# Performance work log

Measured on AMD Instinct MI355X. Metric: run time of the kernel, lower is better.

The kernel has to match this reference:

```python
import jax, jax.numpy as jnp
from jax import lax
import numpy as np

H = W = 2048
C = 3
KSIZE = 2
SIGMA = 2.0
ITERATIONS = 2
RADII = (256.0, 768.0)
# with max_displacement=0 all circle centers coincide, so 'close to any circle'
# reduces to distance^2 < max(radius^2)
SRADII_MAX = max(r ** 2 for r in RADII)
SCLEAN_MAX = max(max(r - KSIZE, 0.0) ** 2 for r in RADII)


def _gaussian_blur(x, sigma):
    """skimage.filters.gaussian equivalent: separable gaussian, truncate=4.0,
    mode='nearest' (edge padding), channel_axis=-1 (no blur across channels)."""
    radius = int(4.0 * sigma + 0.5)
    t = np.arange(-radius, radius + 1, dtype=np.float32)
    k = np.exp(-0.5 * (t / sigma) ** 2)
    k = (k / k.sum()).astype(np.float32)
    for axis in (0, 1):
        pad = [(0, 0)] * x.ndim
        pad[axis] = (radius, radius)
        xp = jnp.pad(x, pad, mode='edge')
        n = x.shape[axis]
        acc = jnp.zeros_like(x)
        for j in range(k.shape[0]):
            acc = acc + k[j] * lax.slice_in_dim(xp, j, j + n, axis=axis)
        x = acc
    return x


def _glass_forward(img, offsets):
    r = KSIZE
    Hv = H - 2 * r + 1  # loop range(r, H-r+1) -> H-2r+1 rows
    Wv = W - 2 * r + 1
    HWtot = H * W
    # original quirk: cx = shape[0]//2 compared against column index w,
    # cy = shape[1]//2 against row index h; identical for a square image.
    cx = H // 2
    cy = W // 2
    ys = jnp.arange(r, H - r + 1)
    xs = jnp.arange(r, W - r + 1)
    HH, WW = jnp.meshgrid(ys, xs, indexing='ij')  # (Hv, Wv)
    d2 = (cx - WW) ** 2 + (cy - HH) ** 2
    swap_mask = (d2 >= SRADII_MAX).reshape(-1)  # swap only OUTSIDE all circles
    local = ((HH - r) * Wv + (WW - r)).reshape(-1)  # raster order within loop
    lin = (HH * W + WW).reshape(-1)

    # Every read in the original swap loop comes from array_orig (never
    # updated), so the final value of each pixel equals array_orig[source]
    # where source is determined by the LAST write targeting that pixel.
    # Each loop step emits two ordered writes:
    #   array[h, w]   = orig[h_, w_]   (order = 2*raster)
    #   array[h_, w_] = orig[h, w]    (order = 2*raster + 1)
    # We replay this exactly with a scatter-max over write order.
    writes = []
    for i in range(ITERATIONS):
        dh = offsets[i, :, :, 0]
        dw = offsets[i, :, :, 1]
        lin_ = ((HH + dh) * W + (WW + dw)).reshape(-1)
        base = i * 2 * Hv * Wv
        o1 = base + 2 * local
        o2 = o1 + 1
        writes.append((lin, lin_, o1))
        writes.append((lin_, lin, o2))

    win = jnp.full((HWtot,), -1, jnp.int32)
    for tgt, src_idx, order in writes:
        win = win.at[tgt].max(jnp.where(swap_mask, order, -1))
    src = jnp.full((HWtot,), -1, jnp.int32)
    for tgt, src_idx, order in writes:
        hit = swap_mask & (order == win[tgt])
        src = src.at[tgt].max(jnp.where(hit, src_idx, -1))

    orig_flat = img.reshape(HWtot, C)
    gathered = orig_flat[jnp.maximum(src, 0)]
    swapped = jnp.where((src >= 0)[:, None], gathered, orig_flat).reshape(H, W, C)

    blurred = jnp.clip(_gaussian_blur(swapped / 255.0, SIGMA), 0.0, 1.0) * 255.0

    # restore original pixels close to the shrunken (clean) circles
    clean = d2 < SCLEAN_MAX  # (Hv, Wv)
    clean_full = jnp.zeros((H, W), bool).at[r:H - r + 1, r:W - r + 1].set(clean)
    return jnp.where(clean_full[:, :, None], img, blurred)


def setup_inputs() -> dict:
    key = jax.random.key(0)
    k1, k2 = jax.random.split(key)
    img = jax.random.uniform(k1, (H, W, C), jnp.float32) * 255.0
    offsets = jax.random.randint(
        k2, (ITERATIONS, H - 2 * KSIZE + 1, W - 2 * KSIZE + 1, 2),
        -KSIZE, KSIZE, dtype=jnp.int32)
    return {"img": img, "offsets": offsets}


def reference(img, offsets):
    return _glass_forward(img, offsets)
```

## Files before the change

### kernel.cpp

```cpp
#include <hip/hip_runtime.h>
#include <hip/hip_fp16.h>

#define Hh 2048
#define Ww 2048
#define HW (2048 * 2048)
constexpr int REG = 2045;
constexpr int RBASE = 2 * 2045 * 2045;
constexpr int SWAP_D2 = 589824;
constexpr int CLEAN_D2 = 586756;

__device__ __constant__ float GK[17] = {
    6.691628e-05f, 4.363490e-04f, 2.215963e-03f, 8.764304e-03f,
    2.699596e-02f, 6.475994e-02f, 1.209875e-01f, 1.760358e-01f,
    1.9947466e-01f, 1.760358e-01f, 1.209875e-01f, 6.475994e-02f,
    2.699596e-02f, 8.764304e-03f, 2.215963e-03f, 4.363490e-04f,
    6.691628e-05f};

constexpr int TX = 32, TY = 8;
constexpr int HX = TX + 3, HY = TY + 3;

__global__ __launch_bounds__(256) void swap_gather(
    const float* __restrict__ img, const int* __restrict__ off,
    __half* __restrict__ A) {
  int x0 = blockIdx.x * TX, y0 = blockIdx.y * TY;
  int tx = threadIdx.x & 31, ty = threadIdx.x >> 5;
  int px = x0 + tx, py = y0 + ty;
  int plin = py * Ww + px;
  int srcoff = 0;

  int mxx = max(abs(1024 - (x0 - 1)), abs(1024 - (x0 + TX + 1)));
  int mxy = max(abs(1024 - (y0 - 1)), abs(1024 - (y0 + TY + 1)));
  if (mxx * mxx + mxy * mxy >= SWAP_D2) {
    __shared__ unsigned sh[HY * HX];
    for (int e = threadIdx.x; e < HY * HX; e += 256) {
      int ly = e / HX, lx = e - ly * HX;
      int qy = y0 - 1 + ly, qx = x0 - 1 + lx;
      unsigned v = 0xFFFFFFFFu;
      int dcx = 1024 - qx, dcy = 1024 - qy;
      if (qy >= 2 && qy <= 2046 && qx >= 2 && qx <= 2046 &&
          dcx * dcx + dcy * dcy >= SWAP_D2) {
        int base = ((qy - 2) * REG + (qx - 2)) * 2;
        const int2 a0 = *(const int2*)&off[base];
        const int2 a1 = *(const int2*)&off[RBASE + base];
        v = (unsigned)(a0.y + 2) | ((unsigned)(a0.x + 2) << 8) |
            ((unsigned)(a1.y + 2) << 16) | ((unsigned)(a1.x + 2) << 24);
      }
      sh[e] = v;
    }
    __syncthreads();

    unsigned w[4][4];
#pragma unroll
    for (int dyi = 0; dyi < 4; ++dyi)
#pragma unroll
      for (int dxi = 0; dxi < 4; ++dxi)
        w[dyi][dxi] = sh[(ty + dyi) * HX + (tx + dxi)];

#define CANDC(dyi, dxi) ((unsigned)((1 - (dxi)) + 2) | ((unsigned)((1 - (dyi)) + 2) << 8))
#define OFFC(dyi, dxi) (-(1 - (dyi)) * Ww - (1 - (dxi)))
#define CAND0(dyi, dxi) \
  if ((w[dyi][dxi] & 0xFFFFu) == CANDC(dyi, dxi)) srcoff = OFFC(dyi, dxi);
#define CAND1(dyi, dxi) \
  if ((w[dyi][dxi] >> 16) == CANDC(dyi, dxi)) srcoff = OFFC(dyi, dxi);

    CAND0(0, 0) CAND0(0, 1) CAND0(0, 2) CAND0(0, 3)
    CAND0(1, 0) CAND0(1, 1) CAND0(1, 2) CAND0(1, 3)
    CAND0(2, 0) CAND0(2, 1) CAND0(2, 2) CAND0(2, 3)
    CAND0(3, 0) CAND0(3, 1) CAND0(3, 2) CAND0(3, 3)
    CAND1(0, 0) CAND1(0, 1) CAND1(0, 2) CAND1(0, 3)
    CAND1(1, 0)
    {
      unsigned wc = w[1][1];
      if ((wc >> 24) != 0xFFu) {
        int dh1 = (int)((wc >> 24) & 0xFFu) - 2;
        int dw1 = (int)((wc >> 16) & 0xFFu) - 2;
        srcoff = dh1 * Ww + dw1;
      }
    }
    CAND1(1, 1) CAND1(1, 2) CAND1(1, 3)
    CAND1(2, 0) CAND1(2, 1) CAND1(2, 2) CAND1(2, 3)
    CAND1(3, 0) CAND1(3, 1) CAND1(3, 2) CAND1(3, 3)
#undef CANDC
#undef OFFC
#undef CAND0
#undef CAND1
  }

  int src = plin + srcoff;
  float r = img[src * 3 + 0];
  float g = img[src * 3 + 1];
  float b = img[src * 3 + 2];
  A[plin] = __float2half(r);
  A[HW + plin] = __float2half(g);
  A[2 * HW + plin] = __float2half(b);
}

constexpr int YPT = 16;
__global__ __launch_bounds__(256) void vblur(const __half* __restrict__ A,
                                             __half* __restrict__ B) {
  int b = blockIdx.x;
  int xcd = b & 7, r = b >> 3;
  int ystrip = (xcd << 4) | (r & 15);
  int rem = r >> 4;
  int xb = rem & 1, c = rem >> 1;
  int x0 = (xb * 256 + threadIdx.x) * 4;
  int y0 = ystrip * YPT;
  const __half* Ap = A + (size_t)c * HW;
  __half* Bp = B + (size_t)c * HW;

  float acc[YPT][4];
#pragma unroll
  for (int k = 0; k < YPT; ++k)
#pragma unroll
    for (int q = 0; q < 4; ++q) acc[k][q] = 0.f;

#pragma unroll
  for (int j = 0; j < YPT + 16; ++j) {
    int ys = y0 - 8 + j;
    ys = ys < 0 ? 0 : (ys > Hh - 1 ? Hh - 1 : ys);
    uint2 raw = *(const uint2*)&Ap[(size_t)ys * Ww + x0];
    __half2 h01 = *(__half2*)&raw.x;
    __half2 h23 = *(__half2*)&raw.y;
    float2 v01 = __half22float2(h01);
    float2 v23 = __half22float2(h23);
#pragma unroll
    for (int k = 0; k < YPT; ++k) {
      int t = j - k;
      if (t >= 0 && t <= 16) {
        float gk = GK[t];
        acc[k][0] += gk * v01.x;
        acc[k][1] += gk * v01.y;
        acc[k][2] += gk * v23.x;
        acc[k][3] += gk * v23.y;
      }
    }
  }
#pragma unroll
  for (int k = 0; k < YPT; ++k) {
    uint2 o;
    __half2 h01 = __float22half2_rn(make_float2(acc[k][0], acc[k][1]));
    __half2 h23 = __float22half2_rn(make_float2(acc[k][2], acc[k][3]));
    o.x = *(unsigned*)&h01;
    o.y = *(unsigned*)&h23;
    *(uint2*)&Bp[(size_t)(y0 + k) * Ww + x0] = o;
  }
}

__global__ __launch_bounds__(256) void hblur_compose(
    const __half* __restrict__ B, const float* __restrict__ img,
    float* __restrict__ out) {
  __shared__ float tile[528 + 1];
  int tid = threadIdx.x;
  int xs = blockIdx.x * 512;
  int y = blockIdx.y;
  float br[3][2];

  for (int c = 0; c < 3; ++c) {
    const __half* Bp = B + (size_t)c * HW + (size_t)y * Ww;
    __syncthreads();
    for (int e = tid; e < 264; e += 256) {
      int xg = xs - 8 + 2 * e;
      float2 v;
      if (xg >= 0 && xg + 1 <= Ww - 1) {
        __half2 h = *(const __half2*)&Bp[xg];
        v = __half22float2(h);
      } else {
        int xlo = xg < 0 ? 0 : (xg > Ww - 1 ? Ww - 1 : xg);
        int xhi = xg + 1 < 0 ? 0 : (xg + 1 > Ww - 1 ? Ww - 1 : xg + 1);
        v = make_float2(__half2float(Bp[xlo]), __half2float(Bp[xhi]));
      }
      *(float2*)&tile[2 * e] = v;
    }
    __syncthreads();
    float f[19];
#pragma unroll
    for (int j = 0; j < 19; ++j) f[j] = tile[2 * tid + j];
    float s0 = 0.f, s1 = 0.f;
#pragma unroll
    for (int j = 0; j < 17; ++j) {
      s0 += GK[j] * f[j];
      s1 += GK[j] * f[j + 1];
    }
    br[c][0] = s0;
    br[c][1] = s1;
  }

  int x = xs + 2 * tid;
#pragma unroll
  for (int u = 0; u < 2; ++u) {
    int xu = x + u;
    int dx = 1024 - xu, dy = 1024 - y;
    bool clean = (xu >= 2 && xu <= 2046 && y >= 2 && y <= 2046 &&
                  dx * dx + dy * dy < CLEAN_D2);
    int p3 = (y * Ww + xu) * 3;
    if (clean) {
      out[p3 + 0] = img[p3 + 0];
      out[p3 + 1] = img[p3 + 1];
      out[p3 + 2] = img[p3 + 2];
    } else {
#pragma unroll
      for (int c = 0; c < 3; ++c) {
        float v = br[c][u];
        v = v < 0.f ? 0.f : (v > 255.f ? 255.f : v);
        out[p3 + c] = v;
      }
    }
  }
}

extern "C" void kernel_launch(void* const* d_in, const int* in_sizes, int n_in,
                              void* d_out, int out_size, void* d_ws,
                              size_t ws_size, hipStream_t stream) {
  const float* img = (const float*)d_in[0];
  const int* off = (const int*)d_in[1];
  float* out = (float*)d_out;

  __half* A = (__half*)d_ws;
  __half* Bp = A + (size_t)3 * HW;

  swap_gather<<<dim3(Ww / TX, Hh / TY), 256, 0, stream>>>(img, off, A);
  vblur<<<768, 256, 0, stream>>>(A, Bp);
  hblur_compose<<<dim3(Ww / 512, Hh), 256, 0, stream>>>(Bp, img, out);
}
```

Measured before the change: 178.9 us.

## Fuse vertical and horizontal blur into one tiled kernel and skip clean tiles

```diff
diff --git a/kernel.cpp b/kernel.cpp
--- a/kernel.cpp
+++ b/kernel.cpp
@@ -8,6 +8,7 @@
 constexpr int RBASE = 2 * 2045 * 2045;
 constexpr int SWAP_D2 = 589824;
 constexpr int CLEAN_D2 = 586756;
+constexpr int SKIP_D2 = 569000;
 
 __device__ __constant__ float GK[17] = {
     6.691628e-05f, 4.363490e-04f, 2.215963e-03f, 8.764304e-03f,
@@ -16,22 +17,31 @@
     2.699596e-02f, 8.764304e-03f, 2.215963e-03f, 4.363490e-04f,
     6.691628e-05f};
 
+__device__ __forceinline__ int clampi(int v, int lo, int hi) {
+  return v < lo ? lo : (v > hi ? hi : v);
+}
+
 constexpr int TX = 32, TY = 8;
 constexpr int HX = TX + 3, HY = TY + 3;
 
 __global__ __launch_bounds__(256) void swap_gather(
     const float* __restrict__ img, const int* __restrict__ off,
     __half* __restrict__ A) {
+  __shared__ unsigned sh[HY * HX];
+  __shared__ __align__(16) float simg[12 * 108];
   int x0 = blockIdx.x * TX, y0 = blockIdx.y * TY;
   int tx = threadIdx.x & 31, ty = threadIdx.x >> 5;
   int px = x0 + tx, py = y0 + ty;
   int plin = py * Ww + px;
-  int srcoff = 0;
-
+
+  int bxx = max(abs(1024 - x0), abs(1024 - (x0 + TX - 1)));
+  int bxy = max(abs(1024 - y0), abs(1024 - (y0 + TY - 1)));
+  if (bxx * bxx + bxy * bxy < SKIP_D2) return;
+
+  float r, g, b;
   int mxx = max(abs(1024 - (x0 - 1)), abs(1024 - (x0 + TX + 1)));
   int mxy = max(abs(1024 - (y0 - 1)), abs(1024 - (y0 + TY + 1)));
   if (mxx * mxx + mxy * mxy >= SWAP_D2) {
-    __shared__ unsigned sh[HY * HX];
     for (int e = threadIdx.x; e < HY * HX; e += 256) {
       int ly = e / HX, lx = e - ly * HX;
       int qy = y0 - 1 + ly, qx = x0 - 1 + lx;
@@ -47,6 +57,23 @@
       }
       sh[e] = v;
     }
+    if (x0 >= 2 && x0 <= 2013) {
+      for (int e = threadIdx.x; e < 648; e += 256) {
+        int rr = e / 54, c2 = e - rr * 54;
+        int qy = clampi(y0 - 2 + rr, 0, 2047);
+        *(float2*)&simg[rr * 108 + 2 * c2] =
+            *(const float2*)&img[(size_t)qy * 6144 + (size_t)(x0 - 2) * 3 +
+                                 2 * c2];
+      }
+    } else {
+      for (int e = threadIdx.x; e < 1296; e += 256) {
+        int rr = e / 108, c3 = e - rr * 108;
+        int col = c3 / 3, ch = c3 - col * 3;
+        int qy = clampi(y0 - 2 + rr, 0, 2047);
+        int qx = clampi(x0 - 2 + col, 0, 2047);
+        simg[e] = img[((size_t)qy * Ww + qx) * 3 + ch];
+      }
+    }
     __syncthreads();
 
     unsigned w[4][4];
@@ -56,12 +83,13 @@
       for (int dxi = 0; dxi < 4; ++dxi)
         w[dyi][dxi] = sh[(ty + dyi) * HX + (tx + dxi)];
 
+    int loff = 0;
 #define CANDC(dyi, dxi) ((unsigned)((1 - (dxi)) + 2) | ((unsigned)((1 - (dyi)) + 2) << 8))
-#define OFFC(dyi, dxi) (-(1 - (dyi)) * Ww - (1 - (dxi)))
+#define LOFFC(dyi, dxi) (-(1 - (dyi)) * 36 - (1 - (dxi)))
 #define CAND0(dyi, dxi) \
-  if ((w[dyi][dxi] & 0xFFFFu) == CANDC(dyi, dxi)) srcoff = OFFC(dyi, dxi);
+  if ((w[dyi][dxi] & 0xFFFFu) == CANDC(dyi, dxi)) loff = LOFFC(dyi, dxi);
 #define CAND1(dyi, dxi) \
-  if ((w[dyi][dxi] >> 16) == CANDC(dyi, dxi)) srcoff = OFFC(dyi, dxi);
+  if ((w[dyi][dxi] >> 16) == CANDC(dyi, dxi)) loff = LOFFC(dyi, dxi);
 
     CAND0(0, 0) CAND0(0, 1) CAND0(0, 2) CAND0(0, 3)
     CAND0(1, 0) CAND0(1, 1) CAND0(1, 2) CAND0(1, 3)
@@ -74,135 +102,124 @@
       if ((wc >> 24) != 0xFFu) {
         int dh1 = (int)((wc >> 24) & 0xFFu) - 2;
         int dw1 = (int)((wc >> 16) & 0xFFu) - 2;
-        srcoff = dh1 * Ww + dw1;
+        loff = dh1 * 36 + dw1;
       }
     }
     CAND1(1, 1) CAND1(1, 2) CAND1(1, 3)
     CAND1(2, 0) CAND1(2, 1) CAND1(2, 2) CAND1(2, 3)
     CAND1(3, 0) CAND1(3, 1) CAND1(3, 2) CAND1(3, 3)
 #undef CANDC
-#undef OFFC
+#undef LOFFC
 #undef CAND0
 #undef CAND1
+
+    int L = ((ty + 2) * 36 + (tx + 2) + loff) * 3;
+    r = simg[L + 0];
+    g = simg[L + 1];
+    b = simg[L + 2];
+  } else {
+    r = img[(size_t)plin * 3 + 0];
+    g = img[(size_t)plin * 3 + 1];
+    b = img[(size_t)plin * 3 + 2];
   }
-
-  int src = plin + srcoff;
-  float r = img[src * 3 + 0];
-  float g = img[src * 3 + 1];
-  float b = img[src * 3 + 2];
   A[plin] = __float2half(r);
   A[HW + plin] = __float2half(g);
   A[2 * HW + plin] = __float2half(b);
 }
 
-constexpr int YPT = 16;
-__global__ __launch_bounds__(256) void vblur(const __half* __restrict__ A,
-                                             __half* __restrict__ B) {
-  int b = blockIdx.x;
-  int xcd = b & 7, r = b >> 3;
-  int ystrip = (xcd << 4) | (r & 15);
-  int rem = r >> 4;
-  int xb = rem & 1, c = rem >> 1;
-  int x0 = (xb * 256 + threadIdx.x) * 4;
-  int y0 = ystrip * YPT;
-  const __half* Ap = A + (size_t)c * HW;
-  __half* Bp = B + (size_t)c * HW;
-
-  float acc[YPT][4];
-#pragma unroll
-  for (int k = 0; k < YPT; ++k)
-#pragma unroll
-    for (int q = 0; q < 4; ++q) acc[k][q] = 0.f;
-
-#pragma unroll
-  for (int j = 0; j < YPT + 16; ++j) {
-    int ys = y0 - 8 + j;
-    ys = ys < 0 ? 0 : (ys > Hh - 1 ? Hh - 1 : ys);
-    uint2 raw = *(const uint2*)&Ap[(size_t)ys * Ww + x0];
-    __half2 h01 = *(__half2*)&raw.x;
-    __half2 h23 = *(__half2*)&raw.y;
-    float2 v01 = __half22float2(h01);
-    float2 v23 = __half22float2(h23);
-#pragma unroll
-    for (int k = 0; k < YPT; ++k) {
-      int t = j - k;
-      if (t >= 0 && t <= 16) {
-        float gk = GK[t];
-        acc[k][0] += gk * v01.x;
-        acc[k][1] += gk * v01.y;
-        acc[k][2] += gk * v23.x;
-        acc[k][3] += gk * v23.y;
-      }
-    }
+constexpr int BTW = 128, BTH = 32;
+constexpr int SW = BTW + 16;
+constexpr int SH = BTH + 16;
+
+__global__ __launch_bounds__(256) void blur_compose(
+    const __half* __restrict__ A, const float* __restrict__ img,
+    float* __restrict__ out) {
+  int lin = blockIdx.x;
+  int swz = (lin & 7) * 128 + (lin >> 3);
+  int tyb = swz & 63, txb = swz >> 6;
+  int x0 = txb * BTW, y0 = tyb * BTH;
+  int tid = threadIdx.x;
+
+  int mxx = max(abs(1024 - x0), abs(1024 - (x0 + BTW - 1)));
+  int mxy = max(abs(1024 - y0), abs(1024 - (y0 + BTH - 1)));
+  if (mxx * mxx + mxy * mxy < CLEAN_D2) {
+    const float4* ip = (const float4*)(img + ((size_t)y0 * Ww + x0) * 3);
+    float4* op = (float4*)(out + ((size_t)y0 * Ww + x0) * 3);
+    for (int e = tid; e < 3072; e += 256) {
+      int rr = e / 96, c4 = e - rr * 96;
+      op[(size_t)rr * 1536 + c4] = ip[(size_t)rr * 1536 + c4];
+    }
+    return;
   }
-#pragma unroll
-  for (int k = 0; k < YPT; ++k) {
-    uint2 o;
-    __half2 h01 = __float22half2_rn(make_float2(acc[k][0], acc[k][1]));
-    __half2 h23 = __float22half2_rn(make_float2(acc[k][2], acc[k][3]));
-    o.x = *(unsigned*)&h01;
-    o.y = *(unsigned*)&h23;
-    *(uint2*)&Bp[(size_t)(y0 + k) * Ww + x0] = o;
-  }
-}
-
-__global__ __launch_bounds__(256) void hblur_compose(
-    const __half* __restrict__ B, const float* __restrict__ img,
-    float* __restrict__ out) {
-  __shared__ float tile[528 + 1];
-  int tid = threadIdx.x;
-  int xs = blockIdx.x * 512;
-  int y = blockIdx.y;
-  float br[3][2];
+
+  __shared__ __align__(16) __half S[SH * SW];
+  __shared__ __align__(8) __half V[BTH * SW];
+
+  bool xin = (x0 >= 8) && (x0 + SW - 8 <= Ww);
 
   for (int c = 0; c < 3; ++c) {
-    const __half* Bp = B + (size_t)c * HW + (size_t)y * Ww;
-    __syncthreads();
-    for (int e = tid; e < 264; e += 256) {
-      int xg = xs - 8 + 2 * e;
-      float2 v;
-      if (xg >= 0 && xg + 1 <= Ww - 1) {
-        __half2 h = *(const __half2*)&Bp[xg];
-        v = __half22float2(h);
-      } else {
-        int xlo = xg < 0 ? 0 : (xg > Ww - 1 ? Ww - 1 : xg);
-        int xhi = xg + 1 < 0 ? 0 : (xg + 1 > Ww - 1 ? Ww - 1 : xg + 1);
-        v = make_float2(__half2float(Bp[xlo]), __half2float(Bp[xhi]));
-      }
-      *(float2*)&tile[2 * e] = v;
-    }
-    __syncthreads();
-    float f[19];
-#pragma unroll
-    for (int j = 0; j < 19; ++j) f[j] = tile[2 * tid + j];
-    float s0 = 0.f, s1 = 0.f;
-#pragma unroll
-    for (int j = 0; j < 17; ++j) {
-      s0 += GK[j] * f[j];
-      s1 += GK[j] * f[j + 1];
-    }
-    br[c][0] = s0;
-    br[c][1] = s1;
-  }
-
-  int x = xs + 2 * tid;
-#pragma unroll
-  for (int u = 0; u < 2; ++u) {
-    int xu = x + u;
-    int dx = 1024 - xu, dy = 1024 - y;
-    bool clean = (xu >= 2 && xu <= 2046 && y >= 2 && y <= 2046 &&
-                  dx * dx + dy * dy < CLEAN_D2);
-    int p3 = (y * Ww + xu) * 3;
-    if (clean) {
-      out[p3 + 0] = img[p3 + 0];
-      out[p3 + 1] = img[p3 + 1];
-      out[p3 + 2] = img[p3 + 2];
+    const __half* Ap = A + (size_t)c * HW;
+    __syncthreads();
+    if (xin) {
+      for (int e = tid; e < SH * 18; e += 256) {
+        int rr = e / 18, ch = e - rr * 18;
+        int ys = clampi(y0 - 8 + rr, 0, Hh - 1);
+        *(uint4*)&S[rr * SW + ch * 8] =
+            *(const uint4*)&Ap[(size_t)ys * Ww + (x0 - 8) + ch * 8];
+      }
     } else {
-#pragma unroll
-      for (int c = 0; c < 3; ++c) {
-        float v = br[c][u];
+      for (int e = tid; e < SH * SW; e += 256) {
+        int rr = e / SW, j = e - rr * SW;
+        int ys = clampi(y0 - 8 + rr, 0, Hh - 1);
+        int xs = clampi(x0 - 8 + j, 0, Ww - 1);
+        S[e] = Ap[(size_t)ys * Ww + xs];
+      }
+    }
+    __syncthreads();
+    for (int e = tid; e < BTH * 72; e += 256) {
+      int rr = e / 72, p = e - rr * 72;
+      float s0 = 0.f, s1 = 0.f;
+#pragma unroll
+      for (int t = 0; t < 17; ++t) {
+        float2 v = __half22float2(*(const __half2*)&S[(rr + t) * SW + 2 * p]);
+        s0 += GK[t] * v.x;
+        s1 += GK[t] * v.y;
+      }
+      *(__half2*)&V[rr * SW + 2 * p] = __float22half2_rn(make_float2(s0, s1));
+    }
+    __syncthreads();
+    for (int e = tid; e < BTH * 64; e += 256) {
+      int rr = e >> 6, xh = e & 63;
+      int x = 2 * xh;
+      float f[18];
+#pragma unroll
+      for (int t = 0; t < 9; ++t) {
+        float2 v = __half22float2(*(const __half2*)&V[rr * SW + x + 2 * t]);
+        f[2 * t] = v.x;
+        f[2 * t + 1] = v.y;
+      }
+      float s0 = 0.f, s1 = 0.f;
+#pragma unroll
+      for (int t = 0; t < 17; ++t) {
+        s0 += GK[t] * f[t];
+        s1 += GK[t] * f[t + 1];
+      }
+      int y = y0 + rr;
+      int xg = x0 + x;
+      int dy = 1024 - y;
+#pragma unroll
+      for (int u = 0; u < 2; ++u) {
+        int xu = xg + u;
+        int dx = 1024 - xu;
+        bool clean = (xu >= 2 && xu <= 2046 && y >= 2 && y <= 2046 &&
+                      dx * dx + dy * dy < CLEAN_D2);
+        int p3 = (y * Ww + xu) * 3 + c;
+        float v = u ? s1 : s0;
         v = v < 0.f ? 0.f : (v > 255.f ? 255.f : v);
-        out[p3 + c] = v;
+        if (clean)
+          out[p3] = img[p3];
+        else
+          out[p3] = v;
       }
     }
   }
@@ -216,9 +233,7 @@
   float* out = (float*)d_out;
 
   __half* A = (__half*)d_ws;
-  __half* Bp = A + (size_t)3 * HW;
 
   swap_gather<<<dim3(Ww / TX, Hh / TY), 256, 0, stream>>>(img, off, A);
-  vblur<<<768, 256, 0, stream>>>(A, Bp);
-  hblur_compose<<<dim3(Ww / 512, Hh), 256, 0, stream>>>(Bp, img, out);
-}
+  blur_compose<<<1024, 256, 0, stream>>>(A, img, out);
+}
```

Result: slower. 203.3 us (+13.7%).
